# Kernel optimization log

Hardware: AMD Instinct MI355X
Metric: run time of the kernel (lower is better)

Reference implementation:

```python
import jax, jax.numpy as jnp
import numpy as np

N_FREQS = 12  # tcnn Frequency encoding n_frequencies


def frequency_encode(x):
    # x: [N, 2] -> [N, 2 * N_FREQS * 2] = [N, 48]
    # NeRF-style: per input dim, per freq j: sin(pi * 2^j * x), cos(pi * 2^j * x)
    freqs = (2.0 ** jnp.arange(N_FREQS, dtype=x.dtype)) * jnp.pi  # [12]
    phase = x[:, :, None] * freqs[None, None, :]                  # [N, 2, 12]
    enc = jnp.concatenate([jnp.sin(phase), jnp.cos(phase)], axis=-1)  # [N, 2, 24]
    return enc.reshape(x.shape[0], -1)                            # [N, 48]


def setup_inputs() -> dict:
    key = jax.random.key(0)
    k0, k1, k2, k3 = jax.random.split(key, 4)
    N = 2097152
    x = jax.random.uniform(k0, (N, 2), dtype=jnp.float32)
    # bias-free FullyFusedMLP weights, width 32, 2 hidden layers
    W0 = jax.random.normal(k1, (48, 32), dtype=jnp.float32) * (1.0 / np.sqrt(48))
    W1 = jax.random.normal(k2, (32, 32), dtype=jnp.float32) * (1.0 / np.sqrt(32))
    W2 = jax.random.normal(k3, (32, 1), dtype=jnp.float32) * (1.0 / np.sqrt(32))
    return {"x": x, "W0": W0, "W1": W1, "W2": W2}


def reference(x, W0, W1, W2):
    h = frequency_encode(x)          # [N, 48]
    h = jnp.sin(h @ W0)              # Sine activation, [N, 32]
    h = jnp.sin(h @ W1)              # [N, 32]
    out = h @ W2                     # no output activation, [N, 1]
    return out.astype(jnp.float32)
```

## Files before the change

kernel.cpp:

```cpp
#include <hip/hip_runtime.h>
#include <hip/hip_bf16.h>
#include <hip/hip_fp16.h>


typedef _Float16 half8 __attribute__((ext_vector_type(8)));
typedef __fp16 fp16x2 __attribute__((ext_vector_type(2)));
typedef float f32x16 __attribute__((ext_vector_type(16)));

#define THREADS 256
#define INV2PI 0.15915494309189535f

__device__ __forceinline__ unsigned packh(float lo, float hi) {
    union { fp16x2 h; unsigned u; } v;
    v.h = __builtin_amdgcn_cvt_pkrtz(lo, hi);
    return v.u;
}

__device__ __forceinline__ unsigned packh_rne(float lo, float hi) {
    union { _Float16 h[2]; unsigned u; } v;
    v.h[0] = (_Float16)lo;
    v.h[1] = (_Float16)hi;
    return v.u;
}

__device__ __forceinline__ void enc_chain(float xd, float sv[12], float cv[12]) {
    sv[0] = __builtin_amdgcn_sinf(xd * 0.5f);
    cv[0] = __builtin_amdgcn_cosf(xd * 0.5f);
#pragma unroll
    for (int j = 1; j < 6; ++j) {
        float t = sv[j - 1] + sv[j - 1];
        sv[j] = t * cv[j - 1];
        cv[j] = fmaf(-t, sv[j - 1], 1.0f);
    }
    sv[6] = __builtin_amdgcn_sinf(xd * 32.0f);
    cv[6] = __builtin_amdgcn_cosf(xd * 32.0f);
#pragma unroll
    for (int j = 7; j < 12; ++j) {
        float t = sv[j - 1] + sv[j - 1];
        sv[j] = t * cv[j - 1];
        cv[j] = fmaf(-t, sv[j - 1], 1.0f);
    }
}

__global__ void build_frags(const float* __restrict__ W0,
                            const float* __restrict__ W1,
                            const float* __restrict__ W2,
                            uint4* __restrict__ ws) {
    int l = threadIdx.x;
    if (l >= 64) return;
    int h = l >> 5, c = l & 31;

#pragma unroll
    for (int t = 0; t < 3; ++t) {
        float ev[8];
#pragma unroll
        for (int e = 0; e < 8; ++e) ev[e] = W0[(h * 24 + 8 * t + e) * 32 + c] * INV2PI;
        ws[t * 64 + l] = make_uint4(packh_rne(ev[0], ev[1]), packh_rne(ev[2], ev[3]),
                                    packh_rne(ev[4], ev[5]), packh_rne(ev[6], ev[7]));
    }
#pragma unroll
    for (int t = 0; t < 2; ++t) {
        float ev[8];
#pragma unroll
        for (int e = 0; e < 8; ++e) {
            int k = (e & 3) + 8 * (e >> 2) + 4 * h + 16 * t;
            ev[e] = W1[k * 32 + c] * INV2PI;
        }
        ws[(3 + t) * 64 + l] = make_uint4(packh_rne(ev[0], ev[1]), packh_rne(ev[2], ev[3]),
                                          packh_rne(ev[4], ev[5]), packh_rne(ev[6], ev[7]));
    }
#pragma unroll
    for (int s = 0; s < 2; ++s)
#pragma unroll
        for (int t = 0; t < 2; ++t) {
            float ev[8];
#pragma unroll
            for (int e = 0; e < 8; ++e) {
                int k = (e & 3) + 8 * (e >> 2) + 4 * h + 16 * t;
                ev[e] = (c == 4 * s) ? W2[k] : 0.0f;
            }
            ws[(5 + 2 * s + t) * 64 + l] = make_uint4(packh_rne(ev[0], ev[1]), packh_rne(ev[2], ev[3]),
                                                      packh_rne(ev[4], ev[5]), packh_rne(ev[6], ev[7]));
        }
}

__global__ __launch_bounds__(THREADS, 4) void siren_mfma_kernel(
    const float* __restrict__ xf,
    const uint4* __restrict__ wf,
    float* __restrict__ out,
    int n)
{
    const int lane = threadIdx.x & 63;
    const int wid = threadIdx.x >> 6;
    const int q = lane & 31, h = lane >> 5;
    const int p0 = blockIdx.x * THREADS + wid * 64;
    if (p0 >= n) return;

    const float xd0 = xf[(p0 + q) * 2 + h];
    const float xd1 = xf[(p0 + 32 + q) * 2 + h];

    union U { uint4 u; half8 v; };
    half8 a0[3], a1[2], d0[2], d1[2];
#pragma unroll
    for (int t = 0; t < 3; ++t) { U tt; tt.u = wf[t * 64 + lane]; a0[t] = tt.v; }
#pragma unroll
    for (int t = 0; t < 2; ++t) { U tt; tt.u = wf[(3 + t) * 64 + lane]; a1[t] = tt.v; }
#pragma unroll
    for (int t = 0; t < 2; ++t) { U tt; tt.u = wf[(5 + t) * 64 + lane]; d0[t] = tt.v; }
#pragma unroll
    for (int t = 0; t < 2; ++t) { U tt; tt.u = wf[(7 + t) * 64 + lane]; d1[t] = tt.v; }

    f32x16 zacc;
#pragma unroll
    for (int i = 0; i < 16; ++i) zacc[i] = 0.0f;

    union F { unsigned u[4]; half8 v; };

    F bf00, bf01, bf02;
    {
        float sv[12], cv[12];
        enc_chain(xd0, sv, cv);
        bf00.u[0] = packh(sv[0], sv[1]);  bf00.u[1] = packh(sv[2], sv[3]);
        bf00.u[2] = packh(sv[4], sv[5]);  bf00.u[3] = packh(sv[6], sv[7]);
        bf01.u[0] = packh(sv[8], sv[9]);  bf01.u[1] = packh(sv[10], sv[11]);
        bf01.u[2] = packh(cv[0], cv[1]);  bf01.u[3] = packh(cv[2], cv[3]);
        bf02.u[0] = packh(cv[4], cv[5]);  bf02.u[1] = packh(cv[6], cv[7]);
        bf02.u[2] = packh(cv[8], cv[9]);  bf02.u[3] = packh(cv[10], cv[11]);
    }
    f32x16 accA;
    accA = __builtin_amdgcn_mfma_f32_32x32x16_f16(a0[0], bf00.v, zacc, 0, 0, 0);
    accA = __builtin_amdgcn_mfma_f32_32x32x16_f16(a0[1], bf01.v, accA, 0, 0, 0);
    accA = __builtin_amdgcn_mfma_f32_32x32x16_f16(a0[2], bf02.v, accA, 0, 0, 0);

    F bf10, bf11, bf12;
    {
        float sv[12], cv[12];
        enc_chain(xd1, sv, cv);
        bf10.u[0] = packh(sv[0], sv[1]);  bf10.u[1] = packh(sv[2], sv[3]);
        bf10.u[2] = packh(sv[4], sv[5]);  bf10.u[3] = packh(sv[6], sv[7]);
        bf11.u[0] = packh(sv[8], sv[9]);  bf11.u[1] = packh(sv[10], sv[11]);
        bf11.u[2] = packh(cv[0], cv[1]);  bf11.u[3] = packh(cv[2], cv[3]);
        bf12.u[0] = packh(cv[4], cv[5]);  bf12.u[1] = packh(cv[6], cv[7]);
        bf12.u[2] = packh(cv[8], cv[9]);  bf12.u[3] = packh(cv[10], cv[11]);
    }
    f32x16 accB;
    accB = __builtin_amdgcn_mfma_f32_32x32x16_f16(a0[0], bf10.v, zacc, 0, 0, 0);
    accB = __builtin_amdgcn_mfma_f32_32x32x16_f16(a0[1], bf11.v, accB, 0, 0, 0);
    accB = __builtin_amdgcn_mfma_f32_32x32x16_f16(a0[2], bf12.v, accB, 0, 0, 0);

    F b1a0, b1b0;
#pragma unroll
    for (int i = 0; i < 4; ++i)
        b1a0.u[i] = packh(__builtin_amdgcn_sinf(accA[2 * i]),
                          __builtin_amdgcn_sinf(accA[2 * i + 1]));
#pragma unroll
    for (int i = 0; i < 4; ++i)
        b1b0.u[i] = packh(__builtin_amdgcn_sinf(accA[8 + 2 * i]),
                          __builtin_amdgcn_sinf(accA[8 + 2 * i + 1]));
    f32x16 acc1A;
    acc1A = __builtin_amdgcn_mfma_f32_32x32x16_f16(a1[0], b1a0.v, zacc, 0, 0, 0);
    acc1A = __builtin_amdgcn_mfma_f32_32x32x16_f16(a1[1], b1b0.v, acc1A, 0, 0, 0);

    F b1a1, b1b1;
#pragma unroll
    for (int i = 0; i < 4; ++i)
        b1a1.u[i] = packh(__builtin_amdgcn_sinf(accB[2 * i]),
                          __builtin_amdgcn_sinf(accB[2 * i + 1]));
#pragma unroll
    for (int i = 0; i < 4; ++i)
        b1b1.u[i] = packh(__builtin_amdgcn_sinf(accB[8 + 2 * i]),
                          __builtin_amdgcn_sinf(accB[8 + 2 * i + 1]));
    f32x16 acc1B;
    acc1B = __builtin_amdgcn_mfma_f32_32x32x16_f16(a1[0], b1a1.v, zacc, 0, 0, 0);
    acc1B = __builtin_amdgcn_mfma_f32_32x32x16_f16(a1[1], b1b1.v, acc1B, 0, 0, 0);

    F b2a0, b2b0;
#pragma unroll
    for (int i = 0; i < 4; ++i)
        b2a0.u[i] = packh(__builtin_amdgcn_sinf(acc1A[2 * i]),
                          __builtin_amdgcn_sinf(acc1A[2 * i + 1]));
#pragma unroll
    for (int i = 0; i < 4; ++i)
        b2b0.u[i] = packh(__builtin_amdgcn_sinf(acc1A[8 + 2 * i]),
                          __builtin_amdgcn_sinf(acc1A[8 + 2 * i + 1]));
    f32x16 accDA;
    accDA = __builtin_amdgcn_mfma_f32_32x32x16_f16(d0[0], b2a0.v, zacc, 0, 0, 0);
    accDA = __builtin_amdgcn_mfma_f32_32x32x16_f16(d0[1], b2b0.v, accDA, 0, 0, 0);

    F b2a1, b2b1;
#pragma unroll
    for (int i = 0; i < 4; ++i)
        b2a1.u[i] = packh(__builtin_amdgcn_sinf(acc1B[2 * i]),
                          __builtin_amdgcn_sinf(acc1B[2 * i + 1]));
#pragma unroll
    for (int i = 0; i < 4; ++i)
        b2b1.u[i] = packh(__builtin_amdgcn_sinf(acc1B[8 + 2 * i]),
                          __builtin_amdgcn_sinf(acc1B[8 + 2 * i + 1]));
    f32x16 accDB;
    accDB = __builtin_amdgcn_mfma_f32_32x32x16_f16(d1[0], b2a1.v, zacc, 0, 0, 0);
    accDB = __builtin_amdgcn_mfma_f32_32x32x16_f16(d1[1], b2b1.v, accDB, 0, 0, 0);

    out[p0 + 32 * h + q] = h ? accDB[0] : accDA[0];
}

extern "C" void kernel_launch(void* const* d_in, const int* in_sizes, int n_in,
                              void* d_out, int out_size, void* d_ws, size_t ws_size,
                              hipStream_t stream) {
    const float* xf = (const float*)d_in[0];
    const float* W0 = (const float*)d_in[1];
    const float* W1 = (const float*)d_in[2];
    const float* W2 = (const float*)d_in[3];
    float* out = (float*)d_out;
    uint4* ws = (uint4*)d_ws;

    const int n = in_sizes[0] / 2;
    build_frags<<<1, 64, 0, stream>>>(W0, W1, W2, ws);
    const int blocks = (n + THREADS - 1) / THREADS;
    siren_mfma_kernel<<<blocks, THREADS, 0, stream>>>(xf, ws, out, n);
}
```

Before: 30.16 us.

## Convert to persistent waves looping over chunks with prefetched inputs

Launches a fixed grid of 1024 blocks, so each wave walks a contiguous chunk of 64-point tiles. The per-wave weight fragment loads are paid once per chunk instead of once per tile. The next tile's x values are prefetched into registers while the current tile is computed. The final-layer MFMAs are merged into one accumulator so the output store needs no lane select. The risks are lower parallelism, which leaves less latency hiding across waves, and tail imbalance.

```diff
diff --git a/kernel.cpp b/kernel.cpp
--- a/kernel.cpp
+++ b/kernel.cpp
@@ -84,20 +84,22 @@
         }
 }
 
+#define BLOCKS 1024
+
 __global__ __launch_bounds__(THREADS, 4) void siren_mfma_kernel(
     const float* __restrict__ xf,
     const uint4* __restrict__ wf,
     float* __restrict__ out,
-    int n)
+    int n, int chunk)
 {
     const int lane = threadIdx.x & 63;
     const int wid = threadIdx.x >> 6;
     const int q = lane & 31, h = lane >> 5;
-    const int p0 = blockIdx.x * THREADS + wid * 64;
+    const int wgid = blockIdx.x * 4 + wid;
+
+    int p0 = wgid * chunk;
     if (p0 >= n) return;
-
-    const float xd0 = xf[(p0 + q) * 2 + h];
-    const float xd1 = xf[(p0 + 32 + q) * 2 + h];
+    const int pend = min(p0 + chunk, n);
 
     union U { uint4 u; half8 v; };
     half8 a0[3], a1[2], d0[2], d1[2];
@@ -116,91 +118,100 @@
 
     union F { unsigned u[4]; half8 v; };
 
-    F bf00, bf01, bf02;
-    {
-        float sv[12], cv[12];
-        enc_chain(xd0, sv, cv);
-        bf00.u[0] = packh(sv[0], sv[1]);  bf00.u[1] = packh(sv[2], sv[3]);
-        bf00.u[2] = packh(sv[4], sv[5]);  bf00.u[3] = packh(sv[6], sv[7]);
-        bf01.u[0] = packh(sv[8], sv[9]);  bf01.u[1] = packh(sv[10], sv[11]);
-        bf01.u[2] = packh(cv[0], cv[1]);  bf01.u[3] = packh(cv[2], cv[3]);
-        bf02.u[0] = packh(cv[4], cv[5]);  bf02.u[1] = packh(cv[6], cv[7]);
-        bf02.u[2] = packh(cv[8], cv[9]);  bf02.u[3] = packh(cv[10], cv[11]);
-    }
-    f32x16 accA;
-    accA = __builtin_amdgcn_mfma_f32_32x32x16_f16(a0[0], bf00.v, zacc, 0, 0, 0);
-    accA = __builtin_amdgcn_mfma_f32_32x32x16_f16(a0[1], bf01.v, accA, 0, 0, 0);
-    accA = __builtin_amdgcn_mfma_f32_32x32x16_f16(a0[2], bf02.v, accA, 0, 0, 0);
-
-    F bf10, bf11, bf12;
-    {
-        float sv[12], cv[12];
-        enc_chain(xd1, sv, cv);
-        bf10.u[0] = packh(sv[0], sv[1]);  bf10.u[1] = packh(sv[2], sv[3]);
-        bf10.u[2] = packh(sv[4], sv[5]);  bf10.u[3] = packh(sv[6], sv[7]);
-        bf11.u[0] = packh(sv[8], sv[9]);  bf11.u[1] = packh(sv[10], sv[11]);
-        bf11.u[2] = packh(cv[0], cv[1]);  bf11.u[3] = packh(cv[2], cv[3]);
-        bf12.u[0] = packh(cv[4], cv[5]);  bf12.u[1] = packh(cv[6], cv[7]);
-        bf12.u[2] = packh(cv[8], cv[9]);  bf12.u[3] = packh(cv[10], cv[11]);
-    }
-    f32x16 accB;
-    accB = __builtin_amdgcn_mfma_f32_32x32x16_f16(a0[0], bf10.v, zacc, 0, 0, 0);
-    accB = __builtin_amdgcn_mfma_f32_32x32x16_f16(a0[1], bf11.v, accB, 0, 0, 0);
-    accB = __builtin_amdgcn_mfma_f32_32x32x16_f16(a0[2], bf12.v, accB, 0, 0, 0);
-
-    F b1a0, b1b0;
-#pragma unroll
-    for (int i = 0; i < 4; ++i)
-        b1a0.u[i] = packh(__builtin_amdgcn_sinf(accA[2 * i]),
-                          __builtin_amdgcn_sinf(accA[2 * i + 1]));
-#pragma unroll
-    for (int i = 0; i < 4; ++i)
-        b1b0.u[i] = packh(__builtin_amdgcn_sinf(accA[8 + 2 * i]),
-                          __builtin_amdgcn_sinf(accA[8 + 2 * i + 1]));
-    f32x16 acc1A;
-    acc1A = __builtin_amdgcn_mfma_f32_32x32x16_f16(a1[0], b1a0.v, zacc, 0, 0, 0);
-    acc1A = __builtin_amdgcn_mfma_f32_32x32x16_f16(a1[1], b1b0.v, acc1A, 0, 0, 0);
-
-    F b1a1, b1b1;
-#pragma unroll
-    for (int i = 0; i < 4; ++i)
-        b1a1.u[i] = packh(__builtin_amdgcn_sinf(accB[2 * i]),
-                          __builtin_amdgcn_sinf(accB[2 * i + 1]));
-#pragma unroll
-    for (int i = 0; i < 4; ++i)
-        b1b1.u[i] = packh(__builtin_amdgcn_sinf(accB[8 + 2 * i]),
-                          __builtin_amdgcn_sinf(accB[8 + 2 * i + 1]));
-    f32x16 acc1B;
-    acc1B = __builtin_amdgcn_mfma_f32_32x32x16_f16(a1[0], b1a1.v, zacc, 0, 0, 0);
-    acc1B = __builtin_amdgcn_mfma_f32_32x32x16_f16(a1[1], b1b1.v, acc1B, 0, 0, 0);
-
-    F b2a0, b2b0;
-#pragma unroll
-    for (int i = 0; i < 4; ++i)
-        b2a0.u[i] = packh(__builtin_amdgcn_sinf(acc1A[2 * i]),
-                          __builtin_amdgcn_sinf(acc1A[2 * i + 1]));
-#pragma unroll
-    for (int i = 0; i < 4; ++i)
-        b2b0.u[i] = packh(__builtin_amdgcn_sinf(acc1A[8 + 2 * i]),
-                          __builtin_amdgcn_sinf(acc1A[8 + 2 * i + 1]));
-    f32x16 accDA;
-    accDA = __builtin_amdgcn_mfma_f32_32x32x16_f16(d0[0], b2a0.v, zacc, 0, 0, 0);
-    accDA = __builtin_amdgcn_mfma_f32_32x32x16_f16(d0[1], b2b0.v, accDA, 0, 0, 0);
-
-    F b2a1, b2b1;
-#pragma unroll
-    for (int i = 0; i < 4; ++i)
-        b2a1.u[i] = packh(__builtin_amdgcn_sinf(acc1B[2 * i]),
-                          __builtin_amdgcn_sinf(acc1B[2 * i + 1]));
-#pragma unroll
-    for (int i = 0; i < 4; ++i)
-        b2b1.u[i] = packh(__builtin_amdgcn_sinf(acc1B[8 + 2 * i]),
-                          __builtin_amdgcn_sinf(acc1B[8 + 2 * i + 1]));
-    f32x16 accDB;
-    accDB = __builtin_amdgcn_mfma_f32_32x32x16_f16(d1[0], b2a1.v, zacc, 0, 0, 0);
-    accDB = __builtin_amdgcn_mfma_f32_32x32x16_f16(d1[1], b2b1.v, accDB, 0, 0, 0);
-
-    out[p0 + 32 * h + q] = h ? accDB[0] : accDA[0];
+    float xa = xf[(p0 + q) * 2 + h];
+    float xb = xf[(p0 + 32 + q) * 2 + h];
+
+    for (int p = p0; p < pend; p += 64) {
+        const int pn = (p + 64 < pend) ? (p + 64) : p;
+        float na = xf[(pn + q) * 2 + h];
+        float nb = xf[(pn + 32 + q) * 2 + h];
+
+        F bf00, bf01, bf02;
+        {
+            float sv[12], cv[12];
+            enc_chain(xa, sv, cv);
+            bf00.u[0] = packh(sv[0], sv[1]);  bf00.u[1] = packh(sv[2], sv[3]);
+            bf00.u[2] = packh(sv[4], sv[5]);  bf00.u[3] = packh(sv[6], sv[7]);
+            bf01.u[0] = packh(sv[8], sv[9]);  bf01.u[1] = packh(sv[10], sv[11]);
+            bf01.u[2] = packh(cv[0], cv[1]);  bf01.u[3] = packh(cv[2], cv[3]);
+            bf02.u[0] = packh(cv[4], cv[5]);  bf02.u[1] = packh(cv[6], cv[7]);
+            bf02.u[2] = packh(cv[8], cv[9]);  bf02.u[3] = packh(cv[10], cv[11]);
+        }
+        f32x16 accA;
+        accA = __builtin_amdgcn_mfma_f32_32x32x16_f16(a0[0], bf00.v, zacc, 0, 0, 0);
+        accA = __builtin_amdgcn_mfma_f32_32x32x16_f16(a0[1], bf01.v, accA, 0, 0, 0);
+        accA = __builtin_amdgcn_mfma_f32_32x32x16_f16(a0[2], bf02.v, accA, 0, 0, 0);
+
+        F bf10, bf11, bf12;
+        {
+            float sv[12], cv[12];
+            enc_chain(xb, sv, cv);
+            bf10.u[0] = packh(sv[0], sv[1]);  bf10.u[1] = packh(sv[2], sv[3]);
+            bf10.u[2] = packh(sv[4], sv[5]);  bf10.u[3] = packh(sv[6], sv[7]);
+            bf11.u[0] = packh(sv[8], sv[9]);  bf11.u[1] = packh(sv[10], sv[11]);
+            bf11.u[2] = packh(cv[0], cv[1]);  bf11.u[3] = packh(cv[2], cv[3]);
+            bf12.u[0] = packh(cv[4], cv[5]);  bf12.u[1] = packh(cv[6], cv[7]);
+            bf12.u[2] = packh(cv[8], cv[9]);  bf12.u[3] = packh(cv[10], cv[11]);
+        }
+        f32x16 accB;
+        accB = __builtin_amdgcn_mfma_f32_32x32x16_f16(a0[0], bf10.v, zacc, 0, 0, 0);
+        accB = __builtin_amdgcn_mfma_f32_32x32x16_f16(a0[1], bf11.v, accB, 0, 0, 0);
+        accB = __builtin_amdgcn_mfma_f32_32x32x16_f16(a0[2], bf12.v, accB, 0, 0, 0);
+
+        F b1a0, b1b0;
+#pragma unroll
+        for (int i = 0; i < 4; ++i)
+            b1a0.u[i] = packh(__builtin_amdgcn_sinf(accA[2 * i]),
+                              __builtin_amdgcn_sinf(accA[2 * i + 1]));
+#pragma unroll
+        for (int i = 0; i < 4; ++i)
+            b1b0.u[i] = packh(__builtin_amdgcn_sinf(accA[8 + 2 * i]),
+                              __builtin_amdgcn_sinf(accA[8 + 2 * i + 1]));
+        f32x16 acc1A;
+        acc1A = __builtin_amdgcn_mfma_f32_32x32x16_f16(a1[0], b1a0.v, zacc, 0, 0, 0);
+        acc1A = __builtin_amdgcn_mfma_f32_32x32x16_f16(a1[1], b1b0.v, acc1A, 0, 0, 0);
+
+        F b1a1, b1b1;
+#pragma unroll
+        for (int i = 0; i < 4; ++i)
+            b1a1.u[i] = packh(__builtin_amdgcn_sinf(accB[2 * i]),
+                              __builtin_amdgcn_sinf(accB[2 * i + 1]));
+#pragma unroll
+        for (int i = 0; i < 4; ++i)
+            b1b1.u[i] = packh(__builtin_amdgcn_sinf(accB[8 + 2 * i]),
+                              __builtin_amdgcn_sinf(accB[8 + 2 * i + 1]));
+        f32x16 acc1B;
+        acc1B = __builtin_amdgcn_mfma_f32_32x32x16_f16(a1[0], b1a1.v, zacc, 0, 0, 0);
+        acc1B = __builtin_amdgcn_mfma_f32_32x32x16_f16(a1[1], b1b1.v, acc1B, 0, 0, 0);
+
+        F b2a0, b2b0, b2a1, b2b1;
+#pragma unroll
+        for (int i = 0; i < 4; ++i)
+            b2a0.u[i] = packh(__builtin_amdgcn_sinf(acc1A[2 * i]),
+                              __builtin_amdgcn_sinf(acc1A[2 * i + 1]));
+#pragma unroll
+        for (int i = 0; i < 4; ++i)
+            b2b0.u[i] = packh(__builtin_amdgcn_sinf(acc1A[8 + 2 * i]),
+                              __builtin_amdgcn_sinf(acc1A[8 + 2 * i + 1]));
+#pragma unroll
+        for (int i = 0; i < 4; ++i)
+            b2a1.u[i] = packh(__builtin_amdgcn_sinf(acc1B[2 * i]),
+                              __builtin_amdgcn_sinf(acc1B[2 * i + 1]));
+#pragma unroll
+        for (int i = 0; i < 4; ++i)
+            b2b1.u[i] = packh(__builtin_amdgcn_sinf(acc1B[8 + 2 * i]),
+                              __builtin_amdgcn_sinf(acc1B[8 + 2 * i + 1]));
+        f32x16 accD;
+        accD = __builtin_amdgcn_mfma_f32_32x32x16_f16(d0[0], b2a0.v, zacc, 0, 0, 0);
+        accD = __builtin_amdgcn_mfma_f32_32x32x16_f16(d0[1], b2b0.v, accD, 0, 0, 0);
+        accD = __builtin_amdgcn_mfma_f32_32x32x16_f16(d1[0], b2a1.v, accD, 0, 0, 0);
+        accD = __builtin_amdgcn_mfma_f32_32x32x16_f16(d1[1], b2b1.v, accD, 0, 0, 0);
+
+        out[p + 32 * h + q] = accD[0];
+
+        xa = na;
+        xb = nb;
+    }
 }
 
 extern "C" void kernel_launch(void* const* d_in, const int* in_sizes, int n_in,
@@ -215,6 +226,9 @@
 
     const int n = in_sizes[0] / 2;
     build_frags<<<1, 64, 0, stream>>>(W0, W1, W2, ws);
-    const int blocks = (n + THREADS - 1) / THREADS;
-    siren_mfma_kernel<<<blocks, THREADS, 0, stream>>>(xf, ws, out, n);
-}
+
+    const int nwaves = BLOCKS * 4;
+    const int tiles = (n + 63) / 64;
+    const int chunk = ((tiles + nwaves - 1) / nwaves) * 64;
+    siren_mfma_kernel<<<BLOCKS, THREADS, 0, stream>>>(xf, ws, out, n, chunk);
+}
```

Measured after the change: 30.74 us. Within noise of the previous version (+1.9%).
